# Kernel tuning notes

Hardware: AMD Instinct MI355X
Metric: run time of the kernel (lower is better)

## Reference

```python
import jax, jax.numpy as jnp
import numpy as np

B, C, H = 32768, 1000, 128


def setup_inputs() -> dict:
    key = jax.random.key(0)
    ks = jax.random.split(key, 4)
    return {
        "logits": jax.random.normal(ks[0], (B, C), dtype=jnp.float32),
        "W1": jax.random.normal(ks[1], (C, H), dtype=jnp.float32) * 0.02,
        "b1": jnp.zeros((H,), dtype=jnp.float32),
        "W2": jax.random.normal(ks[2], (H, H), dtype=jnp.float32) * 0.02,
        "b2": jnp.zeros((H,), dtype=jnp.float32),
        "W3": jax.random.normal(ks[3], (H, C), dtype=jnp.float32) * 0.02,
        "b3": jnp.zeros((C,), dtype=jnp.float32),
    }


def reference(logits, W1, b1, W2, b2, W3, b3):
    prob = jax.nn.softmax(logits, axis=-1)                      # [B, C]
    # descending sort (torch.sort(descending=True))
    order = jnp.argsort(-prob, axis=-1)                          # [B, C] int
    sorted_prob = jnp.take_along_axis(prob, order, axis=-1)      # [B, C]
    # diffs between consecutive sorted probs, last slot = 1
    diffs = jnp.concatenate(
        [sorted_prob[:, :-1] - sorted_prob[:, 1:],
         jnp.ones((prob.shape[0], 1), dtype=prob.dtype)], axis=1)
    # adapter MLP on prob
    h = jax.nn.relu(prob @ W1 + b1)
    h = jax.nn.relu(h @ W2 + b2)
    cal = h @ W3 + b3                                            # [B, C]
    # sigmoid on all but the last column
    cal = jnp.concatenate([jax.nn.sigmoid(cal[:, :-1]), cal[:, -1:]], axis=1)
    v = diffs * cal                                              # [B, C]
    # S.T @ U @ v  ==  scatter(reverse-cumsum(v)) back to original order
    rev_cumsum = jnp.cumsum(v[:, ::-1], axis=1)[:, ::-1]         # suffix sum
    rows = jnp.arange(logits.shape[0])[:, None]
    fitted = jnp.zeros_like(logits).at[rows, order].set(rev_cumsum)
    return fitted + logits
```

## Files before the change

kernel.cpp:

```cpp
#include <hip/hip_runtime.h>
#include <hip/hip_bf16.h>

#define BROWS 32768
#define CDIM 1000
#define CPAD 1024
#define HDIM 128
#define SWZ(w) ((w) ^ ((((w) >> 5) & 7) << 2))

typedef __attribute__((ext_vector_type(8))) short short8;
typedef __attribute__((ext_vector_type(4))) float f32x4;

__device__ inline unsigned short f2bf(float x) {
    unsigned int b = __float_as_uint(x);
    unsigned int r = (b + 0x7FFFu + ((b >> 16) & 1u)) >> 16;
    return (unsigned short)r;
}
__device__ inline float bf2f(unsigned short u) {
    return __uint_as_float(((unsigned int)u) << 16);
}

__global__ __launch_bounds__(256) void k_prep(const float* __restrict__ W1,
                                              const float* __restrict__ W2,
                                              const float* __restrict__ W3,
                                              unsigned short* __restrict__ W1t,
                                              unsigned short* __restrict__ W2t,
                                              unsigned short* __restrict__ W3t) {
    const int idx = blockIdx.x * 256 + threadIdx.x;
    {
        const int n = idx >> 10, k = idx & 1023;
        W1t[idx] = (k < CDIM) ? f2bf(W1[(size_t)k * HDIM + n]) : (unsigned short)0;
    }
    {
        const int n = idx >> 7, k = idx & 127;
        W3t[idx] = (n < CDIM) ? f2bf(W3[(size_t)k * CDIM + n]) : (unsigned short)0;
    }
    if (idx < 16384) {
        const int n = idx >> 7, k = idx & 127;
        W2t[idx] = f2bf(W2[(size_t)k * HDIM + n]);
    }
}

__global__ __launch_bounds__(256) void k_softmax(const float* __restrict__ logits,
                                                 unsigned short* __restrict__ prob) {
    const int wv = threadIdx.x >> 6, lane = threadIdx.x & 63;
    const int row = (blockIdx.x << 2) + wv;
    const int base = lane << 4;
    const float* lrow = logits + (size_t)row * CDIM;
    float lg[16];
#pragma unroll
    for (int q = 0; q < 4; ++q) {
        const int c = base + (q << 2);
        if (c < CDIM) {
            const float4 v4 = *reinterpret_cast<const float4*>(lrow + c);
            lg[q * 4] = v4.x; lg[q * 4 + 1] = v4.y; lg[q * 4 + 2] = v4.z; lg[q * 4 + 3] = v4.w;
        } else {
            lg[q * 4] = lg[q * 4 + 1] = lg[q * 4 + 2] = lg[q * 4 + 3] = -INFINITY;
        }
    }
    float mx = lg[0];
#pragma unroll
    for (int e = 1; e < 16; ++e) mx = fmaxf(mx, lg[e]);
#pragma unroll
    for (int off = 32; off >= 1; off >>= 1) mx = fmaxf(mx, __shfl_xor(mx, off));
    float p[16], s = 0.f;
#pragma unroll
    for (int e = 0; e < 16; ++e) { p[e] = __expf(lg[e] - mx); s += p[e]; }
#pragma unroll
    for (int off = 32; off >= 1; off >>= 1) s += __shfl_xor(s, off);
    const float inv = 1.f / s;
    unsigned int w[8];
#pragma unroll
    for (int i = 0; i < 8; ++i) {
        const unsigned int lo = f2bf(p[2 * i] * inv);
        const unsigned int hi = f2bf(p[2 * i + 1] * inv);
        w[i] = lo | (hi << 16);
    }
    uint4 o0, o1;
    o0.x = w[0]; o0.y = w[1]; o0.z = w[2]; o0.w = w[3];
    o1.x = w[4]; o1.y = w[5]; o1.z = w[6]; o1.w = w[7];
    uint4* dst = reinterpret_cast<uint4*>(prob + (size_t)row * CPAD + base);
    dst[0] = o0; dst[1] = o1;
}

template <int EPI>
__global__ __launch_bounds__(512) void k_gemm(const unsigned short* __restrict__ A, int lda,
                                              const unsigned short* __restrict__ Bt, int ldb,
                                              const float* __restrict__ bias,
                                              unsigned short* __restrict__ outp, int ldo,
                                              int K, int nlimit) {
    __shared__ uint4 As[128 * 8];
    __shared__ uint4 Bs[128 * 8];
    const int tid = threadIdx.x;
    const int bm = blockIdx.x, bn = blockIdx.y;
    const int lane = tid & 63, w = tid >> 6;
    const int wm = (w >> 1) << 5;
    const int wn = (w & 1) << 6;
    const int l15 = lane & 15, l4 = lane >> 4;
    f32x4 acc[2][4] = {};

    for (int k0 = 0; k0 < K; k0 += 64) {
        __syncthreads();
#pragma unroll
        for (int i = 0; i < 2; ++i) {
            const int cid = tid + (i << 9);
            const int r = cid >> 3, c = cid & 7;
            As[(r << 3) + (c ^ (r & 7))] =
                *reinterpret_cast<const uint4*>(A + (size_t)(bm * 128 + r) * lda + k0 + (c << 3));
            Bs[(r << 3) + (c ^ (r & 7))] =
                *reinterpret_cast<const uint4*>(Bt + (size_t)(bn * 128 + r) * ldb + k0 + (c << 3));
        }
        __syncthreads();
#pragma unroll
        for (int kk = 0; kk < 2; ++kk) {
            short8 a[2], b[4];
#pragma unroll
            for (int mf = 0; mf < 2; ++mf) {
                const int r = wm + (mf << 4) + l15;
                a[mf] = *reinterpret_cast<const short8*>(&As[(r << 3) + (((kk << 2) + l4) ^ (r & 7))]);
            }
#pragma unroll
            for (int nf = 0; nf < 4; ++nf) {
                const int r = wn + (nf << 4) + l15;
                b[nf] = *reinterpret_cast<const short8*>(&Bs[(r << 3) + (((kk << 2) + l4) ^ (r & 7))]);
            }
#pragma unroll
            for (int mf = 0; mf < 2; ++mf)
#pragma unroll
                for (int nf = 0; nf < 4; ++nf)
                    acc[mf][nf] = __builtin_amdgcn_mfma_f32_16x16x32_bf16(a[mf], b[nf], acc[mf][nf], 0, 0, 0);
        }
    }
#pragma unroll
    for (int mf = 0; mf < 2; ++mf) {
#pragma unroll
        for (int nf = 0; nf < 4; ++nf) {
            const int n = (bn << 7) + wn + (nf << 4) + l15;
            if (EPI == 1 && n >= nlimit) continue;
            const float bv = bias[n];
#pragma unroll
            for (int r = 0; r < 4; ++r) {
                const int m = (bm << 7) + wm + (mf << 4) + (l4 << 2) + r;
                float v = acc[mf][nf][r] + bv;
                if (EPI == 0) {
                    v = fmaxf(v, 0.f);
                } else {
                    if (n != nlimit - 1) v = 1.f / (1.f + __expf(-v));
                }
                outp[(size_t)m * ldo + n] = f2bf(v);
            }
        }
    }
}

__global__ __launch_bounds__(256) void k_sortfinish(const float* __restrict__ logits,
                                                    const unsigned short* __restrict__ cal,
                                                    float* __restrict__ out) {
    __shared__ unsigned int shm[4 * 1024];
    const int wv = threadIdx.x >> 6, lane = threadIdx.x & 63;
    const int row = (blockIdx.x << 2) + wv;
    unsigned int* sm = &shm[wv << 10];
    const int base = lane << 4;

    int cb[4];
#pragma unroll
    for (int j = 0; j < 4; ++j) { const int wd = base + (j << 2); cb[j] = SWZ(wd); }

    {
        uint4 z; z.x = 0; z.y = 0; z.z = 0; z.w = 0;
#pragma unroll
        for (int j = 0; j < 4; ++j) *reinterpret_cast<uint4*>(&sm[cb[j]]) = z;
    }

    const float* lrow = logits + (size_t)row * CDIM;
    float lg[16];
#pragma unroll
    for (int q = 0; q < 4; ++q) {
        const int c = base + (q << 2);
        if (c < CDIM) {
            const float4 v4 = *reinterpret_cast<const float4*>(lrow + c);
            lg[q * 4] = v4.x; lg[q * 4 + 1] = v4.y; lg[q * 4 + 2] = v4.z; lg[q * 4 + 3] = v4.w;
        } else {
            lg[q * 4] = lg[q * 4 + 1] = lg[q * 4 + 2] = lg[q * 4 + 3] = -INFINITY;
        }
    }
    const unsigned short* crow = cal + (size_t)row * CDIM + base;
    const uint4 c0v = *reinterpret_cast<const uint4*>(crow);
    const uint4 c1v = *reinterpret_cast<const uint4*>(crow + 8);

    float mx = lg[0];
#pragma unroll
    for (int e = 1; e < 16; ++e) mx = fmaxf(mx, lg[e]);
#pragma unroll
    for (int off = 32; off >= 1; off >>= 1) mx = fmaxf(mx, __shfl_xor(mx, off));
    float p[16], s = 0.f;
#pragma unroll
    for (int e = 0; e < 16; ++e) { p[e] = __expf(lg[e] - mx); s += p[e]; }
#pragma unroll
    for (int off = 32; off >= 1; off >>= 1) s += __shfl_xor(s, off);
    const float inv = 1.f / s;
#pragma unroll
    for (int e = 0; e < 16; ++e) p[e] *= inv;

    unsigned int offv[16]; int swk[16];
#pragma unroll
    for (int e = 0; e < 16; ++e) {
        const unsigned int key = __float_as_uint(p[e]) >> 20;
        swk[e] = SWZ((int)key);
        offv[e] = (base + e < CDIM) ? atomicAdd(&sm[swk[e]], 1u) : 0u;
    }

    {
        unsigned int c16[16];
#pragma unroll
        for (int j = 0; j < 4; ++j) {
            const uint4 v4 = *reinterpret_cast<const uint4*>(&sm[cb[j]]);
            c16[4 * j] = v4.x; c16[4 * j + 1] = v4.y; c16[4 * j + 2] = v4.z; c16[4 * j + 3] = v4.w;
        }
        unsigned int lsum = 0;
#pragma unroll
        for (int e = 0; e < 16; ++e) lsum += c16[e];
        unsigned int suf = lsum;
#pragma unroll
        for (int off = 1; off < 64; off <<= 1) {
            const unsigned int u = __shfl_down(suf, off);
            if (lane + off < 64) suf += u;
        }
        unsigned int run = suf - lsum;
        unsigned int stv[16];
#pragma unroll
        for (int e = 15; e >= 0; --e) { stv[e] = run; run += c16[e]; }
#pragma unroll
        for (int j = 0; j < 4; ++j) {
            uint4 v4;
            v4.x = stv[4 * j]; v4.y = stv[4 * j + 1]; v4.z = stv[4 * j + 2]; v4.w = stv[4 * j + 3];
            *reinterpret_cast<uint4*>(&sm[cb[j]]) = v4;
        }
    }

    int swr[16];
#pragma unroll
    for (int e = 0; e < 16; ++e) {
        const int rk = (base + e < CDIM) ? (int)(sm[swk[e]] + offv[e]) : 1023;
        swr[e] = SWZ(rk);
    }

#pragma unroll
    for (int e = 0; e < 16; ++e)
        if (base + e < CDIM) sm[swr[e]] = __float_as_uint(p[e]);

    float sp[16];
#pragma unroll
    for (int j = 0; j < 4; ++j) {
        const uint4 v4 = *reinterpret_cast<const uint4*>(&sm[cb[j]]);
        sp[4 * j] = __uint_as_float(v4.x); sp[4 * j + 1] = __uint_as_float(v4.y);
        sp[4 * j + 2] = __uint_as_float(v4.z); sp[4 * j + 3] = __uint_as_float(v4.w);
    }
    const float spn_next = __shfl_down(sp[0], 1);
    const unsigned int cw[8] = {c0v.x, c0v.y, c0v.z, c0v.w, c1v.x, c1v.y, c1v.z, c1v.w};
    float v[16];
#pragma unroll
    for (int e = 0; e < 16; ++e) {
        const int r = base + e;
        const float cv = bf2f((unsigned short)((cw[e >> 1] >> ((e & 1) * 16)) & 0xFFFFu));
        const float spn = (e < 15) ? sp[e + 1] : spn_next;
        float val;
        if (r < CDIM - 1) val = (sp[e] - spn) * cv;
        else if (r == CDIM - 1) val = cv;
        else val = 0.f;
        v[e] = val;
    }
    float lsuf[16], run = 0.f;
#pragma unroll
    for (int e = 15; e >= 0; --e) { run += v[e]; lsuf[e] = run; }
    float pi = run;
#pragma unroll
    for (int off = 1; off < 64; off <<= 1) {
        const float u = __shfl_up(pi, off);
        if (lane >= off) pi += u;
    }
    const float tot = __shfl(pi, 63);
    const float after = tot - pi;

#pragma unroll
    for (int j = 0; j < 4; ++j) {
        uint4 v4;
        v4.x = __float_as_uint(lsuf[4 * j] + after);
        v4.y = __float_as_uint(lsuf[4 * j + 1] + after);
        v4.z = __float_as_uint(lsuf[4 * j + 2] + after);
        v4.w = __float_as_uint(lsuf[4 * j + 3] + after);
        *reinterpret_cast<uint4*>(&sm[cb[j]]) = v4;
    }
    float f[16];
#pragma unroll
    for (int e = 0; e < 16; ++e) f[e] = __uint_as_float(sm[swr[e]]);
#pragma unroll
    for (int q = 0; q < 4; ++q) {
        const int c = base + (q << 2);
        if (c < CDIM) {
            float4 o;
            o.x = lg[q * 4] + f[q * 4];
            o.y = lg[q * 4 + 1] + f[q * 4 + 1];
            o.z = lg[q * 4 + 2] + f[q * 4 + 2];
            o.w = lg[q * 4 + 3] + f[q * 4 + 3];
            *reinterpret_cast<float4*>(out + (size_t)row * CDIM + c) = o;
        }
    }
}

extern "C" void kernel_launch(void* const* d_in, const int* in_sizes, int n_in,
                              void* d_out, int out_size, void* d_ws, size_t ws_size,
                              hipStream_t stream) {
    const float* logits = (const float*)d_in[0];
    const float* W1 = (const float*)d_in[1];
    const float* b1 = (const float*)d_in[2];
    const float* W2 = (const float*)d_in[3];
    const float* b2 = (const float*)d_in[4];
    const float* W3 = (const float*)d_in[5];
    const float* b3 = (const float*)d_in[6];
    float* out = (float*)d_out;

    char* ws = (char*)d_ws;
    unsigned short* prob = (unsigned short*)ws;
    unsigned short* h1   = (unsigned short*)(ws + 67108864);
    unsigned short* h2   = (unsigned short*)(ws + 75497472);
    unsigned short* W1t  = (unsigned short*)(ws + 83886080);
    unsigned short* W2t  = (unsigned short*)(ws + 84148224);
    unsigned short* W3t  = (unsigned short*)(ws + 84180992);
    unsigned short* cal  = prob;

    k_prep<<<512, 256, 0, stream>>>(W1, W2, W3, W1t, W2t, W3t);
    k_softmax<<<BROWS / 4, 256, 0, stream>>>(logits, prob);
    k_gemm<0><<<dim3(BROWS / 128, 1), 512, 0, stream>>>(prob, CPAD, W1t, CPAD, b1, h1, HDIM, CPAD, 0);
    k_gemm<0><<<dim3(BROWS / 128, 1), 512, 0, stream>>>(h1, HDIM, W2t, HDIM, b2, h2, HDIM, HDIM, 0);
    k_gemm<1><<<dim3(BROWS / 128, 8), 512, 0, stream>>>(h2, HDIM, W3t, HDIM, b3, cal, CDIM, HDIM, CDIM);
    k_sortfinish<<<BROWS / 4, 256, 0, stream>>>(logits, cal, out);
}
```

Measured before the change: 177.5 us.

## Fuse softmax, three-layer MLP and sort-finish into one per-row-tile kernel

Replaces the softmax, three GEMM kernels and the sort/finish kernel with one kernel. Each block handles 16 rows: it computes softmax into LDS, runs the three MLP layers with MFMA reading weights directly from global/L2, writes the calibration in LDS, then does the radix-style sort and suffix scan per row. This removes the global round trips for prob, h1, h2 and cal and several launches. In exchange each block re-reads all weights from cache with only M=16 per tile, so MFMA reuse is low, LDS use is higher (about 48KB), and the grid is small at 2048 blocks.

```diff
diff --git a/kernel.cpp b/kernel.cpp
--- a/kernel.cpp
+++ b/kernel.cpp
@@ -40,269 +40,293 @@
     }
 }
 
-__global__ __launch_bounds__(256) void k_softmax(const float* __restrict__ logits,
-                                                 unsigned short* __restrict__ prob) {
-    const int wv = threadIdx.x >> 6, lane = threadIdx.x & 63;
-    const int row = (blockIdx.x << 2) + wv;
+__global__ __launch_bounds__(256) void k_fused(const float* __restrict__ logits,
+                                               const unsigned short* __restrict__ W1t,
+                                               const float* __restrict__ b1,
+                                               const unsigned short* __restrict__ W2t,
+                                               const float* __restrict__ b2,
+                                               const unsigned short* __restrict__ W3t,
+                                               const float* __restrict__ b3,
+                                               float* __restrict__ out) {
+    __shared__ uint4 pcal[16 * 128];
+    __shared__ unsigned int sortbuf[4 * 1024];
+
+    const int tid = threadIdx.x, lane = tid & 63, wv = tid >> 6;
+    const int l15 = lane & 15, l4 = lane >> 4;
+    const int row0 = blockIdx.x << 4;
     const int base = lane << 4;
-    const float* lrow = logits + (size_t)row * CDIM;
-    float lg[16];
-#pragma unroll
-    for (int q = 0; q < 4; ++q) {
-        const int c = base + (q << 2);
-        if (c < CDIM) {
-            const float4 v4 = *reinterpret_cast<const float4*>(lrow + c);
-            lg[q * 4] = v4.x; lg[q * 4 + 1] = v4.y; lg[q * 4 + 2] = v4.z; lg[q * 4 + 3] = v4.w;
-        } else {
-            lg[q * 4] = lg[q * 4 + 1] = lg[q * 4 + 2] = lg[q * 4 + 3] = -INFINITY;
-        }
-    }
-    float mx = lg[0];
-#pragma unroll
-    for (int e = 1; e < 16; ++e) mx = fmaxf(mx, lg[e]);
-#pragma unroll
-    for (int off = 32; off >= 1; off >>= 1) mx = fmaxf(mx, __shfl_xor(mx, off));
-    float p[16], s = 0.f;
-#pragma unroll
-    for (int e = 0; e < 16; ++e) { p[e] = __expf(lg[e] - mx); s += p[e]; }
-#pragma unroll
-    for (int off = 32; off >= 1; off >>= 1) s += __shfl_xor(s, off);
-    const float inv = 1.f / s;
-    unsigned int w[8];
-#pragma unroll
-    for (int i = 0; i < 8; ++i) {
-        const unsigned int lo = f2bf(p[2 * i] * inv);
-        const unsigned int hi = f2bf(p[2 * i + 1] * inv);
-        w[i] = lo | (hi << 16);
-    }
-    uint4 o0, o1;
-    o0.x = w[0]; o0.y = w[1]; o0.z = w[2]; o0.w = w[3];
-    o1.x = w[4]; o1.y = w[5]; o1.z = w[6]; o1.w = w[7];
-    uint4* dst = reinterpret_cast<uint4*>(prob + (size_t)row * CPAD + base);
-    dst[0] = o0; dst[1] = o1;
-}
-
-template <int EPI>
-__global__ __launch_bounds__(512) void k_gemm(const unsigned short* __restrict__ A, int lda,
-                                              const unsigned short* __restrict__ Bt, int ldb,
-                                              const float* __restrict__ bias,
-                                              unsigned short* __restrict__ outp, int ldo,
-                                              int K, int nlimit) {
-    __shared__ uint4 As[128 * 8];
-    __shared__ uint4 Bs[128 * 8];
-    const int tid = threadIdx.x;
-    const int bm = blockIdx.x, bn = blockIdx.y;
-    const int lane = tid & 63, w = tid >> 6;
-    const int wm = (w >> 1) << 5;
-    const int wn = (w & 1) << 6;
-    const int l15 = lane & 15, l4 = lane >> 4;
-    f32x4 acc[2][4] = {};
-
-    for (int k0 = 0; k0 < K; k0 += 64) {
-        __syncthreads();
-#pragma unroll
-        for (int i = 0; i < 2; ++i) {
-            const int cid = tid + (i << 9);
-            const int r = cid >> 3, c = cid & 7;
-            As[(r << 3) + (c ^ (r & 7))] =
-                *reinterpret_cast<const uint4*>(A + (size_t)(bm * 128 + r) * lda + k0 + (c << 3));
-            Bs[(r << 3) + (c ^ (r & 7))] =
-                *reinterpret_cast<const uint4*>(Bt + (size_t)(bn * 128 + r) * ldb + k0 + (c << 3));
-        }
-        __syncthreads();
-#pragma unroll
-        for (int kk = 0; kk < 2; ++kk) {
-            short8 a[2], b[4];
-#pragma unroll
-            for (int mf = 0; mf < 2; ++mf) {
-                const int r = wm + (mf << 4) + l15;
-                a[mf] = *reinterpret_cast<const short8*>(&As[(r << 3) + (((kk << 2) + l4) ^ (r & 7))]);
-            }
-#pragma unroll
-            for (int nf = 0; nf < 4; ++nf) {
-                const int r = wn + (nf << 4) + l15;
-                b[nf] = *reinterpret_cast<const short8*>(&Bs[(r << 3) + (((kk << 2) + l4) ^ (r & 7))]);
-            }
-#pragma unroll
-            for (int mf = 0; mf < 2; ++mf)
-#pragma unroll
-                for (int nf = 0; nf < 4; ++nf)
-                    acc[mf][nf] = __builtin_amdgcn_mfma_f32_16x16x32_bf16(a[mf], b[nf], acc[mf][nf], 0, 0, 0);
-        }
-    }
-#pragma unroll
-    for (int mf = 0; mf < 2; ++mf) {
-#pragma unroll
-        for (int nf = 0; nf < 4; ++nf) {
-            const int n = (bn << 7) + wn + (nf << 4) + l15;
-            if (EPI == 1 && n >= nlimit) continue;
-            const float bv = bias[n];
-#pragma unroll
-            for (int r = 0; r < 4; ++r) {
-                const int m = (bm << 7) + wm + (mf << 4) + (l4 << 2) + r;
-                float v = acc[mf][nf][r] + bv;
-                if (EPI == 0) {
-                    v = fmaxf(v, 0.f);
-                } else {
-                    if (n != nlimit - 1) v = 1.f / (1.f + __expf(-v));
-                }
-                outp[(size_t)m * ldo + n] = f2bf(v);
-            }
-        }
-    }
-}
-
-__global__ __launch_bounds__(256) void k_sortfinish(const float* __restrict__ logits,
-                                                    const unsigned short* __restrict__ cal,
-                                                    float* __restrict__ out) {
-    __shared__ unsigned int shm[4 * 1024];
-    const int wv = threadIdx.x >> 6, lane = threadIdx.x & 63;
-    const int row = (blockIdx.x << 2) + wv;
-    unsigned int* sm = &shm[wv << 10];
-    const int base = lane << 4;
-
+
+    float mxs[4], invs[4];
+#pragma unroll
+    for (int rr = 0; rr < 4; ++rr) {
+        const int r = (wv << 2) + rr;
+        const float* lrow = logits + (size_t)(row0 + r) * CDIM;
+        float lg[16];
+#pragma unroll
+        for (int q = 0; q < 4; ++q) {
+            const int c = base + (q << 2);
+            if (c < CDIM) {
+                const float4 v4 = *reinterpret_cast<const float4*>(lrow + c);
+                lg[q * 4] = v4.x; lg[q * 4 + 1] = v4.y; lg[q * 4 + 2] = v4.z; lg[q * 4 + 3] = v4.w;
+            } else {
+                lg[q * 4] = lg[q * 4 + 1] = lg[q * 4 + 2] = lg[q * 4 + 3] = -INFINITY;
+            }
+        }
+        float mx = lg[0];
+#pragma unroll
+        for (int e = 1; e < 16; ++e) mx = fmaxf(mx, lg[e]);
+#pragma unroll
+        for (int off = 32; off >= 1; off >>= 1) mx = fmaxf(mx, __shfl_xor(mx, off));
+        float p[16], s = 0.f;
+#pragma unroll
+        for (int e = 0; e < 16; ++e) { p[e] = __expf(lg[e] - mx); s += p[e]; }
+#pragma unroll
+        for (int off = 32; off >= 1; off >>= 1) s += __shfl_xor(s, off);
+        const float inv = 1.f / s;
+        mxs[rr] = mx; invs[rr] = inv;
+        unsigned int w[8];
+#pragma unroll
+        for (int i = 0; i < 8; ++i) {
+            const unsigned int lo = f2bf(p[2 * i] * inv);
+            const unsigned int hi = f2bf(p[2 * i + 1] * inv);
+            w[i] = lo | (hi << 16);
+        }
+        uint4 o0, o1;
+        o0.x = w[0]; o0.y = w[1]; o0.z = w[2]; o0.w = w[3];
+        o1.x = w[4]; o1.y = w[5]; o1.z = w[6]; o1.w = w[7];
+        pcal[r * 128 + ((2 * lane) ^ (r & 7))] = o0;
+        pcal[r * 128 + ((2 * lane + 1) ^ (r & 7))] = o1;
+    }
+    __syncthreads();
+
+    {
+        const int wn = wv << 5;
+        f32x4 acc[2] = {};
+#pragma unroll 8
+        for (int kk = 0; kk < 32; ++kk) {
+            const short8 a = *reinterpret_cast<const short8*>(
+                &pcal[l15 * 128 + (((kk << 2) + l4) ^ (l15 & 7))]);
+#pragma unroll
+            for (int nf = 0; nf < 2; ++nf) {
+                const int n = wn + (nf << 4) + l15;
+                const short8 b = *reinterpret_cast<const short8*>(
+                    W1t + (size_t)n * CPAD + (kk << 5) + (l4 << 3));
+                acc[nf] = __builtin_amdgcn_mfma_f32_16x16x32_bf16(a, b, acc[nf], 0, 0, 0);
+            }
+        }
+        unsigned short* h1 = (unsigned short*)sortbuf;
+#pragma unroll
+        for (int nf = 0; nf < 2; ++nf) {
+            const int n = wn + (nf << 4) + l15;
+            const float bv = b1[n];
+#pragma unroll
+            for (int j = 0; j < 4; ++j) {
+                const int m = (l4 << 2) + j;
+                h1[m * 128 + ((((n >> 3) ^ (m & 7))) << 3) + (n & 7)] =
+                    f2bf(fmaxf(acc[nf][j] + bv, 0.f));
+            }
+        }
+    }
+    __syncthreads();
+
+    {
+        const int wn = wv << 5;
+        f32x4 acc[2] = {};
+#pragma unroll
+        for (int kk = 0; kk < 4; ++kk) {
+            const short8 a = *reinterpret_cast<const short8*>(
+                &((const uint4*)sortbuf)[l15 * 16 + (((kk << 2) + l4) ^ (l15 & 7))]);
+#pragma unroll
+            for (int nf = 0; nf < 2; ++nf) {
+                const int n = wn + (nf << 4) + l15;
+                const short8 b = *reinterpret_cast<const short8*>(
+                    W2t + (size_t)n * HDIM + (kk << 5) + (l4 << 3));
+                acc[nf] = __builtin_amdgcn_mfma_f32_16x16x32_bf16(a, b, acc[nf], 0, 0, 0);
+            }
+        }
+        unsigned short* h2 = (unsigned short*)sortbuf + 2048;
+#pragma unroll
+        for (int nf = 0; nf < 2; ++nf) {
+            const int n = wn + (nf << 4) + l15;
+            const float bv = b2[n];
+#pragma unroll
+            for (int j = 0; j < 4; ++j) {
+                const int m = (l4 << 2) + j;
+                h2[m * 128 + ((((n >> 3) ^ (m & 7))) << 3) + (n & 7)] =
+                    f2bf(fmaxf(acc[nf][j] + bv, 0.f));
+            }
+        }
+    }
+    __syncthreads();
+
+    {
+        f32x4 acc3[16] = {};
+#pragma unroll
+        for (int kk = 0; kk < 4; ++kk) {
+            const short8 a = *reinterpret_cast<const short8*>(
+                &((const uint4*)sortbuf)[256 + l15 * 16 + (((kk << 2) + l4) ^ (l15 & 7))]);
+#pragma unroll
+            for (int nf = 0; nf < 16; ++nf) {
+                const int n = (wv << 8) + (nf << 4) + l15;
+                const short8 b = *reinterpret_cast<const short8*>(
+                    W3t + (size_t)n * HDIM + (kk << 5) + (l4 << 3));
+                acc3[nf] = __builtin_amdgcn_mfma_f32_16x16x32_bf16(a, b, acc3[nf], 0, 0, 0);
+            }
+        }
+        unsigned short* calw = (unsigned short*)pcal;
+#pragma unroll
+        for (int nf = 0; nf < 16; ++nf) {
+            const int n = (wv << 8) + (nf << 4) + l15;
+            const float bv = (n < CDIM) ? b3[n] : 0.f;
+#pragma unroll
+            for (int j = 0; j < 4; ++j) {
+                const int m = (l4 << 2) + j;
+                float v = acc3[nf][j] + bv;
+                if (n != CDIM - 1) v = 1.f / (1.f + __expf(-v));
+                calw[m * 1024 + (((n >> 3) ^ (m & 7)) << 3) + (n & 7)] = f2bf(v);
+            }
+        }
+    }
+    __syncthreads();
+
+    unsigned int* sm = &sortbuf[wv << 10];
     int cb[4];
 #pragma unroll
     for (int j = 0; j < 4; ++j) { const int wd = base + (j << 2); cb[j] = SWZ(wd); }
 
-    {
-        uint4 z; z.x = 0; z.y = 0; z.z = 0; z.w = 0;
-#pragma unroll
-        for (int j = 0; j < 4; ++j) *reinterpret_cast<uint4*>(&sm[cb[j]]) = z;
-    }
-
-    const float* lrow = logits + (size_t)row * CDIM;
-    float lg[16];
-#pragma unroll
-    for (int q = 0; q < 4; ++q) {
-        const int c = base + (q << 2);
-        if (c < CDIM) {
-            const float4 v4 = *reinterpret_cast<const float4*>(lrow + c);
-            lg[q * 4] = v4.x; lg[q * 4 + 1] = v4.y; lg[q * 4 + 2] = v4.z; lg[q * 4 + 3] = v4.w;
-        } else {
-            lg[q * 4] = lg[q * 4 + 1] = lg[q * 4 + 2] = lg[q * 4 + 3] = -INFINITY;
-        }
-    }
-    const unsigned short* crow = cal + (size_t)row * CDIM + base;
-    const uint4 c0v = *reinterpret_cast<const uint4*>(crow);
-    const uint4 c1v = *reinterpret_cast<const uint4*>(crow + 8);
-
-    float mx = lg[0];
-#pragma unroll
-    for (int e = 1; e < 16; ++e) mx = fmaxf(mx, lg[e]);
-#pragma unroll
-    for (int off = 32; off >= 1; off >>= 1) mx = fmaxf(mx, __shfl_xor(mx, off));
-    float p[16], s = 0.f;
-#pragma unroll
-    for (int e = 0; e < 16; ++e) { p[e] = __expf(lg[e] - mx); s += p[e]; }
-#pragma unroll
-    for (int off = 32; off >= 1; off >>= 1) s += __shfl_xor(s, off);
-    const float inv = 1.f / s;
-#pragma unroll
-    for (int e = 0; e < 16; ++e) p[e] *= inv;
-
-    unsigned int offv[16]; int swk[16];
-#pragma unroll
-    for (int e = 0; e < 16; ++e) {
-        const unsigned int key = __float_as_uint(p[e]) >> 20;
-        swk[e] = SWZ((int)key);
-        offv[e] = (base + e < CDIM) ? atomicAdd(&sm[swk[e]], 1u) : 0u;
-    }
-
-    {
-        unsigned int c16[16];
+    for (int rr = 0; rr < 4; ++rr) {
+        const int r = (wv << 2) + rr;
+        const int grow = row0 + r;
+
+        {
+            uint4 z; z.x = 0; z.y = 0; z.z = 0; z.w = 0;
+#pragma unroll
+            for (int j = 0; j < 4; ++j) *reinterpret_cast<uint4*>(&sm[cb[j]]) = z;
+        }
+
+        const float* lrow = logits + (size_t)grow * CDIM;
+        float lg[16];
+#pragma unroll
+        for (int q = 0; q < 4; ++q) {
+            const int c = base + (q << 2);
+            if (c < CDIM) {
+                const float4 v4 = *reinterpret_cast<const float4*>(lrow + c);
+                lg[q * 4] = v4.x; lg[q * 4 + 1] = v4.y; lg[q * 4 + 2] = v4.z; lg[q * 4 + 3] = v4.w;
+            } else {
+                lg[q * 4] = lg[q * 4 + 1] = lg[q * 4 + 2] = lg[q * 4 + 3] = -INFINITY;
+            }
+        }
+        const uint4 c0v = pcal[r * 128 + ((2 * lane) ^ (r & 7))];
+        const uint4 c1v = pcal[r * 128 + ((2 * lane + 1) ^ (r & 7))];
+
+        const float mx = mxs[rr], inv = invs[rr];
+        float p[16];
+#pragma unroll
+        for (int e = 0; e < 16; ++e) p[e] = __expf(lg[e] - mx) * inv;
+
+        unsigned int offv[16]; int swk[16];
+#pragma unroll
+        for (int e = 0; e < 16; ++e) {
+            const unsigned int key = __float_as_uint(p[e]) >> 20;
+            swk[e] = SWZ((int)key);
+            offv[e] = (base + e < CDIM) ? atomicAdd(&sm[swk[e]], 1u) : 0u;
+        }
+
+        {
+            unsigned int c16[16];
+#pragma unroll
+            for (int j = 0; j < 4; ++j) {
+                const uint4 v4 = *reinterpret_cast<const uint4*>(&sm[cb[j]]);
+                c16[4 * j] = v4.x; c16[4 * j + 1] = v4.y; c16[4 * j + 2] = v4.z; c16[4 * j + 3] = v4.w;
+            }
+            unsigned int lsum = 0;
+#pragma unroll
+            for (int e = 0; e < 16; ++e) lsum += c16[e];
+            unsigned int suf = lsum;
+#pragma unroll
+            for (int off = 1; off < 64; off <<= 1) {
+                const unsigned int u = __shfl_down(suf, off);
+                if (lane + off < 64) suf += u;
+            }
+            unsigned int run = suf - lsum;
+            unsigned int stv[16];
+#pragma unroll
+            for (int e = 15; e >= 0; --e) { stv[e] = run; run += c16[e]; }
+#pragma unroll
+            for (int j = 0; j < 4; ++j) {
+                uint4 v4;
+                v4.x = stv[4 * j]; v4.y = stv[4 * j + 1]; v4.z = stv[4 * j + 2]; v4.w = stv[4 * j + 3];
+                *reinterpret_cast<uint4*>(&sm[cb[j]]) = v4;
+            }
+        }
+
+        int swr[16];
+#pragma unroll
+        for (int e = 0; e < 16; ++e) {
+            const int rk = (base + e < CDIM) ? (int)(sm[swk[e]] + offv[e]) : 1023;
+            swr[e] = SWZ(rk);
+        }
+
+#pragma unroll
+        for (int e = 0; e < 16; ++e)
+            if (base + e < CDIM) sm[swr[e]] = __float_as_uint(p[e]);
+
+        float sp[16];
 #pragma unroll
         for (int j = 0; j < 4; ++j) {
             const uint4 v4 = *reinterpret_cast<const uint4*>(&sm[cb[j]]);
-            c16[4 * j] = v4.x; c16[4 * j + 1] = v4.y; c16[4 * j + 2] = v4.z; c16[4 * j + 3] = v4.w;
-        }
-        unsigned int lsum = 0;
-#pragma unroll
-        for (int e = 0; e < 16; ++e) lsum += c16[e];
-        unsigned int suf = lsum;
+            sp[4 * j] = __uint_as_float(v4.x); sp[4 * j + 1] = __uint_as_float(v4.y);
+            sp[4 * j + 2] = __uint_as_float(v4.z); sp[4 * j + 3] = __uint_as_float(v4.w);
+        }
+        const float spn_next = __shfl_down(sp[0], 1);
+        const unsigned int cw[8] = {c0v.x, c0v.y, c0v.z, c0v.w, c1v.x, c1v.y, c1v.z, c1v.w};
+        float v[16];
+#pragma unroll
+        for (int e = 0; e < 16; ++e) {
+            const int rk = base + e;
+            const float cv = bf2f((unsigned short)((cw[e >> 1] >> ((e & 1) * 16)) & 0xFFFFu));
+            const float spn = (e < 15) ? sp[e + 1] : spn_next;
+            float val;
+            if (rk < CDIM - 1) val = (sp[e] - spn) * cv;
+            else if (rk == CDIM - 1) val = cv;
+            else val = 0.f;
+            v[e] = val;
+        }
+        float lsuf[16], run = 0.f;
+#pragma unroll
+        for (int e = 15; e >= 0; --e) { run += v[e]; lsuf[e] = run; }
+        float pi = run;
 #pragma unroll
         for (int off = 1; off < 64; off <<= 1) {
-            const unsigned int u = __shfl_down(suf, off);
-            if (lane + off < 64) suf += u;
-        }
-        unsigned int run = suf - lsum;
-        unsigned int stv[16];
-#pragma unroll
-        for (int e = 15; e >= 0; --e) { stv[e] = run; run += c16[e]; }
+            const float u = __shfl_up(pi, off);
+            if (lane >= off) pi += u;
+        }
+        const float tot = __shfl(pi, 63);
+        const float after = tot - pi;
+
 #pragma unroll
         for (int j = 0; j < 4; ++j) {
             uint4 v4;
-            v4.x = stv[4 * j]; v4.y = stv[4 * j + 1]; v4.z = stv[4 * j + 2]; v4.w = stv[4 * j + 3];
+            v4.x = __float_as_uint(lsuf[4 * j] + after);
+            v4.y = __float_as_uint(lsuf[4 * j + 1] + after);
+            v4.z = __float_as_uint(lsuf[4 * j + 2] + after);
+            v4.w = __float_as_uint(lsuf[4 * j + 3] + after);
             *reinterpret_cast<uint4*>(&sm[cb[j]]) = v4;
         }
-    }
-
-    int swr[16];
-#pragma unroll
-    for (int e = 0; e < 16; ++e) {
-        const int rk = (base + e < CDIM) ? (int)(sm[swk[e]] + offv[e]) : 1023;
-        swr[e] = SWZ(rk);
-    }
-
-#pragma unroll
-    for (int e = 0; e < 16; ++e)
-        if (base + e < CDIM) sm[swr[e]] = __float_as_uint(p[e]);
-
-    float sp[16];
-#pragma unroll
-    for (int j = 0; j < 4; ++j) {
-        const uint4 v4 = *reinterpret_cast<const uint4*>(&sm[cb[j]]);
-        sp[4 * j] = __uint_as_float(v4.x); sp[4 * j + 1] = __uint_as_float(v4.y);
-        sp[4 * j + 2] = __uint_as_float(v4.z); sp[4 * j + 3] = __uint_as_float(v4.w);
-    }
-    const float spn_next = __shfl_down(sp[0], 1);
-    const unsigned int cw[8] = {c0v.x, c0v.y, c0v.z, c0v.w, c1v.x, c1v.y, c1v.z, c1v.w};
-    float v[16];
-#pragma unroll
-    for (int e = 0; e < 16; ++e) {
-        const int r = base + e;
-        const float cv = bf2f((unsigned short)((cw[e >> 1] >> ((e & 1) * 16)) & 0xFFFFu));
-        const float spn = (e < 15) ? sp[e + 1] : spn_next;
-        float val;
-        if (r < CDIM - 1) val = (sp[e] - spn) * cv;
-        else if (r == CDIM - 1) val = cv;
-        else val = 0.f;
-        v[e] = val;
-    }
-    float lsuf[16], run = 0.f;
-#pragma unroll
-    for (int e = 15; e >= 0; --e) { run += v[e]; lsuf[e] = run; }
-    float pi = run;
-#pragma unroll
-    for (int off = 1; off < 64; off <<= 1) {
-        const float u = __shfl_up(pi, off);
-        if (lane >= off) pi += u;
-    }
-    const float tot = __shfl(pi, 63);
-    const float after = tot - pi;
-
-#pragma unroll
-    for (int j = 0; j < 4; ++j) {
-        uint4 v4;
-        v4.x = __float_as_uint(lsuf[4 * j] + after);
-        v4.y = __float_as_uint(lsuf[4 * j + 1] + after);
-        v4.z = __float_as_uint(lsuf[4 * j + 2] + after);
-        v4.w = __float_as_uint(lsuf[4 * j + 3] + after);
-        *reinterpret_cast<uint4*>(&sm[cb[j]]) = v4;
-    }
-    float f[16];
-#pragma unroll
-    for (int e = 0; e < 16; ++e) f[e] = __uint_as_float(sm[swr[e]]);
-#pragma unroll
-    for (int q = 0; q < 4; ++q) {
-        const int c = base + (q << 2);
-        if (c < CDIM) {
-            float4 o;
-            o.x = lg[q * 4] + f[q * 4];
-            o.y = lg[q * 4 + 1] + f[q * 4 + 1];
-            o.z = lg[q * 4 + 2] + f[q * 4 + 2];
-            o.w = lg[q * 4 + 3] + f[q * 4 + 3];
-            *reinterpret_cast<float4*>(out + (size_t)row * CDIM + c) = o;
+        float f[16];
+#pragma unroll
+        for (int e = 0; e < 16; ++e) f[e] = __uint_as_float(sm[swr[e]]);
+#pragma unroll
+        for (int q = 0; q < 4; ++q) {
+            const int c = base + (q << 2);
+            if (c < CDIM) {
+                float4 o;
+                o.x = lg[q * 4] + f[q * 4];
+                o.y = lg[q * 4 + 1] + f[q * 4 + 1];
+                o.z = lg[q * 4 + 2] + f[q * 4 + 2];
+                o.w = lg[q * 4 + 3] + f[q * 4 + 3];
+                *reinterpret_cast<float4*>(out + (size_t)grow * CDIM + c) = o;
+            }
         }
     }
 }
@@ -320,18 +344,10 @@
     float* out = (float*)d_out;
 
     char* ws = (char*)d_ws;
-    unsigned short* prob = (unsigned short*)ws;
-    unsigned short* h1   = (unsigned short*)(ws + 67108864);
-    unsigned short* h2   = (unsigned short*)(ws + 75497472);
-    unsigned short* W1t  = (unsigned short*)(ws + 83886080);
-    unsigned short* W2t  = (unsigned short*)(ws + 84148224);
-    unsigned short* W3t  = (unsigned short*)(ws + 84180992);
-    unsigned short* cal  = prob;
+    unsigned short* W1t = (unsigned short*)ws;
+    unsigned short* W2t = (unsigned short*)(ws + 262144);
+    unsigned short* W3t = (unsigned short*)(ws + 294912);
 
     k_prep<<<512, 256, 0, stream>>>(W1, W2, W3, W1t, W2t, W3t);
-    k_softmax<<<BROWS / 4, 256, 0, stream>>>(logits, prob);
-    k_gemm<0><<<dim3(BROWS / 128, 1), 512, 0, stream>>>(prob, CPAD, W1t, CPAD, b1, h1, HDIM, CPAD, 0);
-    k_gemm<0><<<dim3(BROWS / 128, 1), 512, 0, stream>>>(h1, HDIM, W2t, HDIM, b2, h2, HDIM, HDIM, 0);
-    k_gemm<1><<<dim3(BROWS / 128, 8), 512, 0, stream>>>(h2, HDIM, W3t, HDIM, b3, cal, CDIM, HDIM, CDIM);
-    k_sortfinish<<<BROWS / 4, 256, 0, stream>>>(logits, cal, out);
-}
+    k_fused<<<BROWS / 16, 256, 0, stream>>>(logits, W1t, b1, W2t, b2, W3t, b3, out);
+}
```

Result: slower. 247.4 us (+39.3%).

## Reuse softmax row stats and prefetch next row in sort-finish kernel

Applied to the files above, without the earlier changes.

The softmax kernel now stores each row's max and inverse sum, so the sort-finish kernel rebuilds probabilities directly instead of redoing two wave-wide reductions. Each wave in the sort-finish kernel now handles four consecutive rows. It double-buffers the logits, calibration and stat loads for the next row while sorting the current one, to hide global memory latency. The h1/h2 buffers are merged into one, so the second GEMM reads and writes the same rows in place. The changes cost more registers and launch fewer blocks, which may reduce occupancy.

```diff
diff --git a/kernel.cpp b/kernel.cpp
--- a/kernel.cpp
+++ b/kernel.cpp
@@ -41,7 +41,8 @@
 }
 
 __global__ __launch_bounds__(256) void k_softmax(const float* __restrict__ logits,
-                                                 unsigned short* __restrict__ prob) {
+                                                 unsigned short* __restrict__ prob,
+                                                 float2* __restrict__ rstat) {
     const int wv = threadIdx.x >> 6, lane = threadIdx.x & 63;
     const int row = (blockIdx.x << 2) + wv;
     const int base = lane << 4;
@@ -80,6 +81,7 @@
     o1.x = w[4]; o1.y = w[5]; o1.z = w[6]; o1.w = w[7];
     uint4* dst = reinterpret_cast<uint4*>(prob + (size_t)row * CPAD + base);
     dst[0] = o0; dst[1] = o1;
+    if (lane == 0) rstat[row] = make_float2(mx, inv);
 }
 
 template <int EPI>
@@ -153,156 +155,176 @@
 }
 
 __global__ __launch_bounds__(256) void k_sortfinish(const float* __restrict__ logits,
+                                                    const float2* __restrict__ rstat,
                                                     const unsigned short* __restrict__ cal,
                                                     float* __restrict__ out) {
     __shared__ unsigned int shm[4 * 1024];
     const int wv = threadIdx.x >> 6, lane = threadIdx.x & 63;
-    const int row = (blockIdx.x << 2) + wv;
     unsigned int* sm = &shm[wv << 10];
     const int base = lane << 4;
+    const int row0 = (blockIdx.x << 4) + (wv << 2);
 
     int cb[4];
 #pragma unroll
     for (int j = 0; j < 4; ++j) { const int wd = base + (j << 2); cb[j] = SWZ(wd); }
 
+    float4 lgb[2][4]; uint4 c0b[2], c1b[2]; float2 stb[2];
     {
-        uint4 z; z.x = 0; z.y = 0; z.z = 0; z.w = 0;
-#pragma unroll
-        for (int j = 0; j < 4; ++j) *reinterpret_cast<uint4*>(&sm[cb[j]]) = z;
-    }
-
-    const float* lrow = logits + (size_t)row * CDIM;
-    float lg[16];
-#pragma unroll
-    for (int q = 0; q < 4; ++q) {
-        const int c = base + (q << 2);
-        if (c < CDIM) {
-            const float4 v4 = *reinterpret_cast<const float4*>(lrow + c);
-            lg[q * 4] = v4.x; lg[q * 4 + 1] = v4.y; lg[q * 4 + 2] = v4.z; lg[q * 4 + 3] = v4.w;
-        } else {
-            lg[q * 4] = lg[q * 4 + 1] = lg[q * 4 + 2] = lg[q * 4 + 3] = -INFINITY;
-        }
-    }
-    const unsigned short* crow = cal + (size_t)row * CDIM + base;
-    const uint4 c0v = *reinterpret_cast<const uint4*>(crow);
-    const uint4 c1v = *reinterpret_cast<const uint4*>(crow + 8);
-
-    float mx = lg[0];
-#pragma unroll
-    for (int e = 1; e < 16; ++e) mx = fmaxf(mx, lg[e]);
-#pragma unroll
-    for (int off = 32; off >= 1; off >>= 1) mx = fmaxf(mx, __shfl_xor(mx, off));
-    float p[16], s = 0.f;
-#pragma unroll
-    for (int e = 0; e < 16; ++e) { p[e] = __expf(lg[e] - mx); s += p[e]; }
-#pragma unroll
-    for (int off = 32; off >= 1; off >>= 1) s += __shfl_xor(s, off);
-    const float inv = 1.f / s;
-#pragma unroll
-    for (int e = 0; e < 16; ++e) p[e] *= inv;
-
-    unsigned int offv[16]; int swk[16];
-#pragma unroll
-    for (int e = 0; e < 16; ++e) {
-        const unsigned int key = __float_as_uint(p[e]) >> 20;
-        swk[e] = SWZ((int)key);
-        offv[e] = (base + e < CDIM) ? atomicAdd(&sm[swk[e]], 1u) : 0u;
-    }
-
-    {
-        unsigned int c16[16];
+        const float* lrow = logits + (size_t)row0 * CDIM;
+#pragma unroll
+        for (int q = 0; q < 4; ++q) {
+            const int c = base + (q << 2);
+            lgb[0][q] = (c < CDIM) ? *reinterpret_cast<const float4*>(lrow + c)
+                                   : make_float4(-INFINITY, -INFINITY, -INFINITY, -INFINITY);
+        }
+        const unsigned short* crow = cal + (size_t)row0 * CDIM + base;
+        c0b[0] = *reinterpret_cast<const uint4*>(crow);
+        c1b[0] = *reinterpret_cast<const uint4*>(crow + 8);
+        stb[0] = rstat[row0];
+    }
+
+#pragma unroll
+    for (int rr = 0; rr < 4; ++rr) {
+        const int buf = rr & 1;
+        const int grow = row0 + rr;
+
+        if (rr < 3) {
+            const int nrow = grow + 1;
+            const float* lrow = logits + (size_t)nrow * CDIM;
+#pragma unroll
+            for (int q = 0; q < 4; ++q) {
+                const int c = base + (q << 2);
+                lgb[buf ^ 1][q] = (c < CDIM) ? *reinterpret_cast<const float4*>(lrow + c)
+                                             : make_float4(-INFINITY, -INFINITY, -INFINITY, -INFINITY);
+            }
+            const unsigned short* crow = cal + (size_t)nrow * CDIM + base;
+            c0b[buf ^ 1] = *reinterpret_cast<const uint4*>(crow);
+            c1b[buf ^ 1] = *reinterpret_cast<const uint4*>(crow + 8);
+            stb[buf ^ 1] = rstat[nrow];
+        }
+
+        float lg[16];
+#pragma unroll
+        for (int q = 0; q < 4; ++q) {
+            lg[q * 4] = lgb[buf][q].x; lg[q * 4 + 1] = lgb[buf][q].y;
+            lg[q * 4 + 2] = lgb[buf][q].z; lg[q * 4 + 3] = lgb[buf][q].w;
+        }
+        const unsigned int cw[8] = {c0b[buf].x, c0b[buf].y, c0b[buf].z, c0b[buf].w,
+                                    c1b[buf].x, c1b[buf].y, c1b[buf].z, c1b[buf].w};
+        const float mx = stb[buf].x, inv = stb[buf].y;
+
+        {
+            uint4 z; z.x = 0; z.y = 0; z.z = 0; z.w = 0;
+#pragma unroll
+            for (int j = 0; j < 4; ++j) *reinterpret_cast<uint4*>(&sm[cb[j]]) = z;
+        }
+
+        float p[16];
+#pragma unroll
+        for (int e = 0; e < 16; ++e) p[e] = __expf(lg[e] - mx) * inv;
+
+        unsigned int offv[16]; int swk[16];
+#pragma unroll
+        for (int e = 0; e < 16; ++e) {
+            const unsigned int key = __float_as_uint(p[e]) >> 20;
+            swk[e] = SWZ((int)key);
+            offv[e] = (base + e < CDIM) ? atomicAdd(&sm[swk[e]], 1u) : 0u;
+        }
+
+        {
+            unsigned int c16[16];
+#pragma unroll
+            for (int j = 0; j < 4; ++j) {
+                const uint4 v4 = *reinterpret_cast<const uint4*>(&sm[cb[j]]);
+                c16[4 * j] = v4.x; c16[4 * j + 1] = v4.y; c16[4 * j + 2] = v4.z; c16[4 * j + 3] = v4.w;
+            }
+            unsigned int lsum = 0;
+#pragma unroll
+            for (int e = 0; e < 16; ++e) lsum += c16[e];
+            unsigned int suf = lsum;
+#pragma unroll
+            for (int off = 1; off < 64; off <<= 1) {
+                const unsigned int u = __shfl_down(suf, off);
+                if (lane + off < 64) suf += u;
+            }
+            unsigned int run = suf - lsum;
+            unsigned int stv[16];
+#pragma unroll
+            for (int e = 15; e >= 0; --e) { stv[e] = run; run += c16[e]; }
+#pragma unroll
+            for (int j = 0; j < 4; ++j) {
+                uint4 v4;
+                v4.x = stv[4 * j]; v4.y = stv[4 * j + 1]; v4.z = stv[4 * j + 2]; v4.w = stv[4 * j + 3];
+                *reinterpret_cast<uint4*>(&sm[cb[j]]) = v4;
+            }
+        }
+
+        int swr[16];
+#pragma unroll
+        for (int e = 0; e < 16; ++e) {
+            const int rk = (base + e < CDIM) ? (int)(sm[swk[e]] + offv[e]) : 1023;
+            swr[e] = SWZ(rk);
+        }
+
+#pragma unroll
+        for (int e = 0; e < 16; ++e)
+            if (base + e < CDIM) sm[swr[e]] = __float_as_uint(p[e]);
+
+        float sp[16];
 #pragma unroll
         for (int j = 0; j < 4; ++j) {
             const uint4 v4 = *reinterpret_cast<const uint4*>(&sm[cb[j]]);
-            c16[4 * j] = v4.x; c16[4 * j + 1] = v4.y; c16[4 * j + 2] = v4.z; c16[4 * j + 3] = v4.w;
-        }
-        unsigned int lsum = 0;
-#pragma unroll
-        for (int e = 0; e < 16; ++e) lsum += c16[e];
-        unsigned int suf = lsum;
+            sp[4 * j] = __uint_as_float(v4.x); sp[4 * j + 1] = __uint_as_float(v4.y);
+            sp[4 * j + 2] = __uint_as_float(v4.z); sp[4 * j + 3] = __uint_as_float(v4.w);
+        }
+        const float spn_next = __shfl_down(sp[0], 1);
+        float v[16];
+#pragma unroll
+        for (int e = 0; e < 16; ++e) {
+            const int r = base + e;
+            const float cv = bf2f((unsigned short)((cw[e >> 1] >> ((e & 1) * 16)) & 0xFFFFu));
+            const float spn = (e < 15) ? sp[e + 1] : spn_next;
+            float val;
+            if (r < CDIM - 1) val = (sp[e] - spn) * cv;
+            else if (r == CDIM - 1) val = cv;
+            else val = 0.f;
+            v[e] = val;
+        }
+        float lsuf[16], run = 0.f;
+#pragma unroll
+        for (int e = 15; e >= 0; --e) { run += v[e]; lsuf[e] = run; }
+        float pi = run;
 #pragma unroll
         for (int off = 1; off < 64; off <<= 1) {
-            const unsigned int u = __shfl_down(suf, off);
-            if (lane + off < 64) suf += u;
-        }
-        unsigned int run = suf - lsum;
-        unsigned int stv[16];
-#pragma unroll
-        for (int e = 15; e >= 0; --e) { stv[e] = run; run += c16[e]; }
+            const float u = __shfl_up(pi, off);
+            if (lane >= off) pi += u;
+        }
+        const float tot = __shfl(pi, 63);
+        const float after = tot - pi;
+
 #pragma unroll
         for (int j = 0; j < 4; ++j) {
             uint4 v4;
-            v4.x = stv[4 * j]; v4.y = stv[4 * j + 1]; v4.z = stv[4 * j + 2]; v4.w = stv[4 * j + 3];
+            v4.x = __float_as_uint(lsuf[4 * j] + after);
+            v4.y = __float_as_uint(lsuf[4 * j + 1] + after);
+            v4.z = __float_as_uint(lsuf[4 * j + 2] + after);
+            v4.w = __float_as_uint(lsuf[4 * j + 3] + after);
             *reinterpret_cast<uint4*>(&sm[cb[j]]) = v4;
         }
-    }
-
-    int swr[16];
-#pragma unroll
-    for (int e = 0; e < 16; ++e) {
-        const int rk = (base + e < CDIM) ? (int)(sm[swk[e]] + offv[e]) : 1023;
-        swr[e] = SWZ(rk);
-    }
-
-#pragma unroll
-    for (int e = 0; e < 16; ++e)
-        if (base + e < CDIM) sm[swr[e]] = __float_as_uint(p[e]);
-
-    float sp[16];
-#pragma unroll
-    for (int j = 0; j < 4; ++j) {
-        const uint4 v4 = *reinterpret_cast<const uint4*>(&sm[cb[j]]);
-        sp[4 * j] = __uint_as_float(v4.x); sp[4 * j + 1] = __uint_as_float(v4.y);
-        sp[4 * j + 2] = __uint_as_float(v4.z); sp[4 * j + 3] = __uint_as_float(v4.w);
-    }
-    const float spn_next = __shfl_down(sp[0], 1);
-    const unsigned int cw[8] = {c0v.x, c0v.y, c0v.z, c0v.w, c1v.x, c1v.y, c1v.z, c1v.w};
-    float v[16];
-#pragma unroll
-    for (int e = 0; e < 16; ++e) {
-        const int r = base + e;
-        const float cv = bf2f((unsigned short)((cw[e >> 1] >> ((e & 1) * 16)) & 0xFFFFu));
-        const float spn = (e < 15) ? sp[e + 1] : spn_next;
-        float val;
-        if (r < CDIM - 1) val = (sp[e] - spn) * cv;
-        else if (r == CDIM - 1) val = cv;
-        else val = 0.f;
-        v[e] = val;
-    }
-    float lsuf[16], run = 0.f;
-#pragma unroll
-    for (int e = 15; e >= 0; --e) { run += v[e]; lsuf[e] = run; }
-    float pi = run;
-#pragma unroll
-    for (int off = 1; off < 64; off <<= 1) {
-        const float u = __shfl_up(pi, off);
-        if (lane >= off) pi += u;
-    }
-    const float tot = __shfl(pi, 63);
-    const float after = tot - pi;
-
-#pragma unroll
-    for (int j = 0; j < 4; ++j) {
-        uint4 v4;
-        v4.x = __float_as_uint(lsuf[4 * j] + after);
-        v4.y = __float_as_uint(lsuf[4 * j + 1] + after);
-        v4.z = __float_as_uint(lsuf[4 * j + 2] + after);
-        v4.w = __float_as_uint(lsuf[4 * j + 3] + after);
-        *reinterpret_cast<uint4*>(&sm[cb[j]]) = v4;
-    }
-    float f[16];
-#pragma unroll
-    for (int e = 0; e < 16; ++e) f[e] = __uint_as_float(sm[swr[e]]);
-#pragma unroll
-    for (int q = 0; q < 4; ++q) {
-        const int c = base + (q << 2);
-        if (c < CDIM) {
-            float4 o;
-            o.x = lg[q * 4] + f[q * 4];
-            o.y = lg[q * 4 + 1] + f[q * 4 + 1];
-            o.z = lg[q * 4 + 2] + f[q * 4 + 2];
-            o.w = lg[q * 4 + 3] + f[q * 4 + 3];
-            *reinterpret_cast<float4*>(out + (size_t)row * CDIM + c) = o;
+        float f[16];
+#pragma unroll
+        for (int e = 0; e < 16; ++e) f[e] = __uint_as_float(sm[swr[e]]);
+#pragma unroll
+        for (int q = 0; q < 4; ++q) {
+            const int c = base + (q << 2);
+            if (c < CDIM) {
+                float4 o;
+                o.x = lg[q * 4] + f[q * 4];
+                o.y = lg[q * 4 + 1] + f[q * 4 + 1];
+                o.z = lg[q * 4 + 2] + f[q * 4 + 2];
+                o.w = lg[q * 4 + 3] + f[q * 4 + 3];
+                *reinterpret_cast<float4*>(out + (size_t)grow * CDIM + c) = o;
+            }
         }
     }
 }
@@ -321,17 +343,17 @@
 
     char* ws = (char*)d_ws;
     unsigned short* prob = (unsigned short*)ws;
-    unsigned short* h1   = (unsigned short*)(ws + 67108864);
-    unsigned short* h2   = (unsigned short*)(ws + 75497472);
-    unsigned short* W1t  = (unsigned short*)(ws + 83886080);
-    unsigned short* W2t  = (unsigned short*)(ws + 84148224);
-    unsigned short* W3t  = (unsigned short*)(ws + 84180992);
+    unsigned short* h12  = (unsigned short*)(ws + 67108864);
+    float2*         rstat= (float2*)(ws + 75497472);
+    unsigned short* W1t  = (unsigned short*)(ws + 75759616);
+    unsigned short* W2t  = (unsigned short*)(ws + 76021760);
+    unsigned short* W3t  = (unsigned short*)(ws + 76054528);
     unsigned short* cal  = prob;
 
     k_prep<<<512, 256, 0, stream>>>(W1, W2, W3, W1t, W2t, W3t);
-    k_softmax<<<BROWS / 4, 256, 0, stream>>>(logits, prob);
-    k_gemm<0><<<dim3(BROWS / 128, 1), 512, 0, stream>>>(prob, CPAD, W1t, CPAD, b1, h1, HDIM, CPAD, 0);
-    k_gemm<0><<<dim3(BROWS / 128, 1), 512, 0, stream>>>(h1, HDIM, W2t, HDIM, b2, h2, HDIM, HDIM, 0);
-    k_gemm<1><<<dim3(BROWS / 128, 8), 512, 0, stream>>>(h2, HDIM, W3t, HDIM, b3, cal, CDIM, HDIM, CDIM);
-    k_sortfinish<<<BROWS / 4, 256, 0, stream>>>(logits, cal, out);
-}
+    k_softmax<<<BROWS / 4, 256, 0, stream>>>(logits, prob, rstat);
+    k_gemm<0><<<dim3(BROWS / 128, 1), 512, 0, stream>>>(prob, CPAD, W1t, CPAD, b1, h12, HDIM, CPAD, 0);
+    k_gemm<0><<<dim3(BROWS / 128, 1), 512, 0, stream>>>(h12, HDIM, W2t, HDIM, b2, h12, HDIM, HDIM, 0);
+    k_gemm<1><<<dim3(BROWS / 128, 8), 512, 0, stream>>>(h12, HDIM, W3t, HDIM, b3, cal, CDIM, HDIM, CDIM);
+    k_sortfinish<<<BROWS / 16, 256, 0, stream>>>(logits, rstat, cal, out);
+}
```

New measurement: 177.5 us (median of 2 runs). No clear change (-0.0%).
